# Optimization experiments

Measured on AMD Instinct MI355X. Metric: run time of the kernel, lower is better.

Reference implementation:

```python
import jax, jax.numpy as jnp
import numpy as np

H, P, N, D, T, MLPW, B = 64, 4, 16, 8, 64, 512, 2048
D_IN = 1 + H + P * H  # 321


def _linear_init(key, i, o):
    k1, k2 = jax.random.split(key)
    s = 1.0 / np.sqrt(i)
    W = jax.random.uniform(k1, (i, o), jnp.float32, -s, s)
    b = jax.random.uniform(k2, (o,), jnp.float32, -s, s)
    return W, b


def setup_inputs() -> dict:
    key = jax.random.key(0)
    ks = jax.random.split(key, 10)
    dims_f = [(D_IN, MLPW), (MLPW, MLPW), (MLPW, MLPW), (MLPW, H)]
    dims_g = [(D_IN, MLPW), (MLPW, MLPW), (MLPW, MLPW), (MLPW, H * N)]
    inp = {}
    for idx, (i, o) in enumerate(dims_f):
        W, b = _linear_init(ks[idx], i, o)
        inp[f"fW{idx}"], inp[f"fb{idx}"] = W, b
    for idx, (i, o) in enumerate(dims_g):
        W, b = _linear_init(ks[4 + idx], i, o)
        inp[f"gW{idx}"], inp[f"gb{idx}"] = W, b
    inp["rW"], inp["rb"] = _linear_init(ks[8], H, D)
    inp["ts"] = jnp.arange(T, dtype=jnp.float32)  # uniform grid, dt = 1
    inp["dbt"] = jax.random.normal(ks[9], (T - 1, B, N), jnp.float32)  # per-step randn noise
    inp["batch_size"] = B
    return inp


def _mlp(x, params):
    # Linear+ReLU stack, final Linear with tanh (tscale=1.0)
    for W, b in params[:-1]:
        x = jax.nn.relu(x @ W + b)
    W, b = params[-1]
    return jnp.tanh(x @ W + b)


def _forward(ts, dbt, fp, gp, rW, rb, batch_size):
    x0 = jnp.ones((batch_size, H), jnp.float32)  # fixed=True initial state
    dt = ts[1] - ts[0]  # dt_scale = 1
    hist = jnp.zeros((T, batch_size, H), jnp.float32).at[0].set(x0)
    curr_x, curr_t = x0, ts[0]
    xs = [x0]
    for k in range(T - 1):  # one integration step per output interval (uniform ts)
        # ortho rfft over the growing state history (length k+1); keep first P coeffs,
        # real part (matches torch complex -> .float() cast), zero-pad to P.
        coeffs = jnp.fft.rfft(hist[: k + 1], axis=0, norm="ortho")  # (F, B, H) complex
        c = jnp.real(coeffs[:P]).astype(jnp.float32)
        if c.shape[0] < P:
            c = jnp.concatenate(
                [c, jnp.zeros((P - c.shape[0], batch_size, H), jnp.float32)], axis=0
            )
        feats = jnp.transpose(c, (1, 0, 2)).reshape(batch_size, P * H)  # (B, P*H)
        tcol = jnp.broadcast_to(jnp.reshape(curr_t, (1, 1)), (batch_size, 1))
        tx = jnp.concatenate([tcol, curr_x, feats], axis=1)  # (B, 1+H+P*H)
        drift = _mlp(tx, fp)  # (B, H)
        diff = _mlp(tx, gp).reshape(batch_size, H, N)  # (B, H, N)
        curr_x = curr_x + drift * dt + jnp.einsum("bhn,bn->bh", diff, dbt[k])
        curr_t = jnp.minimum(curr_t + dt, ts[-1])
        hist = hist.at[k + 1].set(curr_x)
        xs.append(curr_x)  # linear_interp degenerates to curr_x on uniform grid
    xs = jnp.stack(xs, axis=1)  # (B, T, H)
    ys = xs @ rW + rb  # readout, (B, T, D)
    tse = jnp.broadcast_to(ts[None, :, None], (batch_size, T, 1))
    # linear_interpolation_coeffs is identity for NaN-free data
    return jnp.concatenate([tse, ys], axis=2)  # (B, T, 1+D)


def reference(fW0, fb0, fW1, fb1, fW2, fb2, fW3, fb3,
              gW0, gb0, gW1, gb1, gW2, gb2, gW3, gb3,
              rW, rb, ts, dbt, batch_size):
    fp = [(fW0, fb0), (fW1, fb1), (fW2, fb2), (fW3, fb3)]
    gp = [(gW0, gb0), (gW1, gb1), (gW2, gb2), (gW3, gb3)]
    return _forward(ts, dbt, fp, gp, rW, rb, batch_size)
```

## Files before the change

### kernel.cpp

```cpp
#include <hip/hip_runtime.h>
#include <math.h>

constexpr int kH   = 64;
constexpr int kP   = 4;
constexpr int kN   = 16;
constexpr int kD   = 8;
constexpr int kT   = 64;
constexpr int kWd  = 512;
constexpr int kB   = 2048;
constexpr int kDIN = 1 + kH + kP * kH;
constexpr int kKP  = 352;
constexpr int kBH  = kB * kH;

typedef __attribute__((ext_vector_type(8))) short short8;
typedef __attribute__((ext_vector_type(4))) float f32x4;

__device__ __forceinline__ short f2bf(float x) {
    union { float f; unsigned u; } v; v.f = x;
    unsigned r = (v.u + 0x7FFFu + ((v.u >> 16) & 1u)) >> 16;
    return (short)r;
}

__device__ __forceinline__ void gload16(const short* g, short* l) {
    __builtin_amdgcn_global_load_lds(
        (const __attribute__((address_space(1))) unsigned int*)g,
        (__attribute__((address_space(3))) unsigned int*)l, 16, 0, 0);
}

__global__ __launch_bounds__(256) void transpose_bf16(const float* __restrict__ W,
                                                      short* __restrict__ Wt,
                                                      int K, int N, int Kp, int Np) {
    int idx = blockIdx.x * 256 + threadIdx.x;
    if (idx >= Kp * Np) return;
    int n = idx / Kp, kk = idx % Kp;
    float v = (kk < K && n < N) ? W[(size_t)kk * N + n] : 0.f;
    Wt[idx] = f2bf(v);
}

__global__ __launch_bounds__(256) void prep_bias(const float* __restrict__ fb0,
                                                 const float* __restrict__ gb0,
                                                 float* __restrict__ b0c) {
    int i = blockIdx.x * 256 + threadIdx.x;
    if (i < 1024) b0c[i] = (i < kWd) ? fb0[i] : gb0[i - kWd];
}

__global__ __launch_bounds__(256) void init_k(float* __restrict__ hist,
                                              short* __restrict__ txh) {
    int idx = blockIdx.x * 256 + threadIdx.x;
    if (idx < kBH) hist[idx] = 1.0f;
    if (idx < kB * (kKP - kDIN)) {
        int b = idx / (kKP - kDIN), c = idx % (kKP - kDIN);
        txh[(size_t)b * kKP + kDIN + c] = 0;
    }
}

__global__ __launch_bounds__(256) void step_pre(float* __restrict__ hist,
                                                const float* __restrict__ drift,
                                                const float* __restrict__ diffb,
                                                const float* __restrict__ dbt,
                                                short* __restrict__ txh, int k) {
    const int L = k + 1;
    __shared__ float ctab[kT * kP];
    int tid = threadIdx.x;
    float invs = rsqrtf((float)L);
    for (int i = tid; i < L * kP; i += 256) {
        int j = i >> 2, p = i & 3;
        ctab[i] = cosf(6.283185307179586f * (float)(p * j) / (float)L) * invs;
    }
    __syncthreads();
    int idx = blockIdx.x * 256 + tid;
    int b = idx >> 6, h = idx & 63;
    float xk;
    if (k == 0) {
        xk = 1.0f;
    } else {
        xk = hist[(size_t)(k - 1) * kBH + idx] + drift[idx];
        const float* dr = diffb + (size_t)b * 1024 + h * kN;
        const float* wr = dbt + (size_t)(k - 1) * kB * kN + b * kN;
#pragma unroll
        for (int n = 0; n < kN; ++n) xk += dr[n] * wr[n];
        hist[(size_t)k * kBH + idx] = xk;
    }
    const float* hp = hist + (size_t)b * kH + h;
    float a0 = 0.f, a1 = 0.f, a2 = 0.f, a3 = 0.f;
    for (int j = 0; j < k; ++j) {
        float x = hp[(size_t)j * kBH];
        a0 += x * ctab[j * 4 + 0];
        a1 += x * ctab[j * 4 + 1];
        a2 += x * ctab[j * 4 + 2];
        a3 += x * ctab[j * 4 + 3];
    }
    a0 += xk * ctab[k * 4 + 0];
    a1 += xk * ctab[k * 4 + 1];
    a2 += xk * ctab[k * 4 + 2];
    a3 += xk * ctab[k * 4 + 3];
    if (L < 2) a1 = 0.f;
    if (L < 4) a2 = 0.f;
    if (L < 6) a3 = 0.f;
    short* th = txh + (size_t)b * kKP;
    th[1 + kH + 0 * kH + h] = f2bf(a0);
    th[1 + kH + 1 * kH + h] = f2bf(a1);
    th[1 + kH + 2 * kH + h] = f2bf(a2);
    th[1 + kH + 3 * kH + h] = f2bf(a3);
    th[1 + h] = f2bf(xk);
    if (h == 0) th[0] = f2bf((float)k);
}

struct MArg {
    const short* A;
    const short* Bt;
    const float* bias;
    short* Cb;
    float* Cf;
    int K, lda, ldc, act, Nw;
};

__global__ __launch_bounds__(256) void gemm_mfma(MArg f, MArg g, int ysplit) {
    const int y = blockIdx.y;
    MArg a;
    int n0;
    if (y < ysplit) { a = f; n0 = y * 64; }
    else            { a = g; n0 = (y - ysplit) * 64; }
    const int m0 = blockIdx.x * 64;

    __shared__ __align__(16) short sA[64 * 32];
    __shared__ __align__(16) short sB[64 * 32];

    const int tid = threadIdx.x;
    const int lane = tid & 63;
    const int w = tid >> 6;
    const int wm = (w & 1) * 32;
    const int wn = (w >> 1) * 32;

    f32x4 acc[2][2] = {};

    const int sr = tid >> 2;
    const int sc = (tid & 3) * 8;
    const short* gA = a.A  + (size_t)(m0 + sr) * a.lda + sc;
    const short* gB = a.Bt + (size_t)(n0 + sr) * a.K + sc;

    for (int k0 = 0; k0 < a.K; k0 += 32) {
        __syncthreads();
        gload16(gA + k0, &sA[sr * 32 + sc]);
        gload16(gB + k0, &sB[sr * 32 + sc]);
        __syncthreads();

        const int fr = lane & 15, kb = (lane >> 4) * 8;
        short8 av[2], bv[2];
#pragma unroll
        for (int i = 0; i < 2; ++i) {
            av[i] = *(const short8*)&sA[(wm + i * 16 + fr) * 32 + kb];
            bv[i] = *(const short8*)&sB[(wn + i * 16 + fr) * 32 + kb];
        }
#pragma unroll
        for (int i = 0; i < 2; ++i)
#pragma unroll
            for (int j = 0; j < 2; ++j)
                acc[i][j] = __builtin_amdgcn_mfma_f32_16x16x32_bf16(av[i], bv[j], acc[i][j], 0, 0, 0);
    }

    const int fr = lane & 15, rq = (lane >> 4) * 4;
#pragma unroll
    for (int j = 0; j < 2; ++j) {
        int n = n0 + wn + j * 16 + fr;
        if (n >= a.Nw) continue;
        float bias = a.bias[n];
#pragma unroll
        for (int i = 0; i < 2; ++i) {
#pragma unroll
            for (int r = 0; r < 4; ++r) {
                int m = m0 + wm + i * 16 + rq + r;
                float v = acc[i][j][r] + bias;
                if (a.act == 0) {
                    a.Cb[(size_t)m * a.ldc + n] = f2bf(fmaxf(v, 0.f));
                } else {
                    a.Cf[(size_t)m * a.ldc + n] = tanhf(v);
                }
            }
        }
    }
}

__global__ __launch_bounds__(256) void update_k(float* __restrict__ hist,
                                                const float* __restrict__ drift,
                                                const float* __restrict__ diffb,
                                                const float* __restrict__ dbt, int k) {
    int idx = blockIdx.x * 256 + threadIdx.x;
    int b = idx >> 6, h = idx & 63;
    float s = hist[(size_t)k * kBH + idx] + drift[idx];
    const float* dr = diffb + (size_t)b * 1024 + h * kN;
    const float* wr = dbt + (size_t)k * kB * kN + b * kN;
#pragma unroll
    for (int n = 0; n < kN; ++n) s += dr[n] * wr[n];
    hist[(size_t)(k + 1) * kBH + idx] = s;
}

__global__ __launch_bounds__(256) void readout_k(const float* __restrict__ hist,
                                                 const float* __restrict__ rW,
                                                 const float* __restrict__ rb,
                                                 const float* __restrict__ ts,
                                                 float* __restrict__ out) {
    __shared__ float sW[kH * kD];
    __shared__ float sb[kD];
    __shared__ float sts[kT];
    int tid = threadIdx.x;
    sW[tid] = rW[tid];
    sW[tid + 256] = rW[tid + 256];
    if (tid < kD) sb[tid] = rb[tid];
    if (tid < kT) sts[tid] = ts[tid];
    __syncthreads();
    int idx = blockIdx.x * 256 + tid;
    int t = idx & (kT - 1), b = idx >> 6;
    const float* xr = hist + (size_t)t * kBH + (size_t)b * kH;
    float acc[kD];
#pragma unroll
    for (int d = 0; d < kD; ++d) acc[d] = sb[d];
    for (int h = 0; h < kH; ++h) {
        float x = xr[h];
#pragma unroll
        for (int d = 0; d < kD; ++d) acc[d] += x * sW[h * kD + d];
    }
    float* o = out + (size_t)((size_t)b * kT + t) * (1 + kD);
    o[0] = sts[t];
#pragma unroll
    for (int d = 0; d < kD; ++d) o[1 + d] = acc[d];
}

extern "C" void kernel_launch(void* const* d_in, const int* in_sizes, int n_in,
                              void* d_out, int out_size, void* d_ws, size_t ws_size,
                              hipStream_t stream) {
    const float* fW0 = (const float*)d_in[0];  const float* fb0 = (const float*)d_in[1];
    const float* fW1 = (const float*)d_in[2];  const float* fb1 = (const float*)d_in[3];
    const float* fW2 = (const float*)d_in[4];  const float* fb2 = (const float*)d_in[5];
    const float* fW3 = (const float*)d_in[6];  const float* fb3 = (const float*)d_in[7];
    const float* gW0 = (const float*)d_in[8];  const float* gb0 = (const float*)d_in[9];
    const float* gW1 = (const float*)d_in[10]; const float* gb1 = (const float*)d_in[11];
    const float* gW2 = (const float*)d_in[12]; const float* gb2 = (const float*)d_in[13];
    const float* gW3 = (const float*)d_in[14]; const float* gb3 = (const float*)d_in[15];
    const float* rW  = (const float*)d_in[16]; const float* rb  = (const float*)d_in[17];
    const float* ts  = (const float*)d_in[18]; const float* dbt = (const float*)d_in[19];
    float* out = (float*)d_out;

    char* p = (char*)d_ws;
    float* hist  = (float*)p;  p += (size_t)kT * kBH * 4;
    float* drift = (float*)p;  p += (size_t)kBH * 4;
    float* diffb = (float*)p;  p += (size_t)kB * 1024 * 4;
    float* b0c   = (float*)p;  p += 1024 * 4;
    short* txh   = (short*)p;  p += (size_t)kB * kKP * 2;
    short* b1h   = (short*)p;  p += (size_t)kB * 1024 * 2;
    short* b2h   = (short*)p;  p += (size_t)kB * 1024 * 2;
    short* W0t   = (short*)p;  p += (size_t)1024 * kKP * 2;
    short* fW1t  = (short*)p;  p += (size_t)512 * 512 * 2;
    short* gW1t  = (short*)p;  p += (size_t)512 * 512 * 2;
    short* fW2t  = (short*)p;  p += (size_t)512 * 512 * 2;
    short* gW2t  = (short*)p;  p += (size_t)512 * 512 * 2;
    short* fW3t  = (short*)p;  p += (size_t)64 * 512 * 2;
    short* gW3t  = (short*)p;  p += (size_t)1024 * 512 * 2;

    auto tgrid = [](int n) { return dim3((n + 255) / 256); };
    transpose_bf16<<<tgrid(kKP * 512), 256, 0, stream>>>(fW0, W0t, kDIN, 512, kKP, 512);
    transpose_bf16<<<tgrid(kKP * 512), 256, 0, stream>>>(gW0, W0t + (size_t)512 * kKP, kDIN, 512, kKP, 512);
    transpose_bf16<<<tgrid(512 * 512), 256, 0, stream>>>(fW1, fW1t, 512, 512, 512, 512);
    transpose_bf16<<<tgrid(512 * 512), 256, 0, stream>>>(gW1, gW1t, 512, 512, 512, 512);
    transpose_bf16<<<tgrid(512 * 512), 256, 0, stream>>>(fW2, fW2t, 512, 512, 512, 512);
    transpose_bf16<<<tgrid(512 * 512), 256, 0, stream>>>(gW2, gW2t, 512, 512, 512, 512);
    transpose_bf16<<<tgrid(512 * 64), 256, 0, stream>>>(fW3, fW3t, 512, 64, 512, 64);
    transpose_bf16<<<tgrid(512 * 1024), 256, 0, stream>>>(gW3, gW3t, 512, 1024, 512, 1024);
    prep_bias<<<dim3(4), 256, 0, stream>>>(fb0, gb0, b0c);
    init_k<<<dim3(kBH / 256), 256, 0, stream>>>(hist, txh);

    for (int k = 0; k < kT - 1; ++k) {
        step_pre<<<dim3(kBH / 256), 256, 0, stream>>>(hist, drift, diffb, dbt, txh, k);

        MArg l1{txh, W0t, b0c, b1h, nullptr, kKP, kKP, 1024, 0, 1024};
        gemm_mfma<<<dim3(32, 16), 256, 0, stream>>>(l1, l1, 16);

        MArg f2{b1h, fW1t, fb1, b2h, nullptr, 512, 1024, 1024, 0, 512};
        MArg g2{b1h + 512, gW1t, gb1, b2h + 512, nullptr, 512, 1024, 1024, 0, 512};
        gemm_mfma<<<dim3(32, 16), 256, 0, stream>>>(f2, g2, 8);

        MArg f3{b2h, fW2t, fb2, b1h, nullptr, 512, 1024, 1024, 0, 512};
        MArg g3{b2h + 512, gW2t, gb2, b1h + 512, nullptr, 512, 1024, 1024, 0, 512};
        gemm_mfma<<<dim3(32, 16), 256, 0, stream>>>(f3, g3, 8);

        MArg f4{b1h, fW3t, fb3, nullptr, drift, 512, 1024, kH, 1, kH};
        MArg g4{b1h + 512, gW3t, gb3, nullptr, diffb, 512, 1024, 1024, 1, 1024};
        gemm_mfma<<<dim3(32, 17), 256, 0, stream>>>(f4, g4, 1);
    }

    update_k<<<dim3(kBH / 256), 256, 0, stream>>>(hist, drift, diffb, dbt, kT - 2);
    readout_k<<<dim3(kB * kT / 256), 256, 0, stream>>>(hist, rW, rb, ts, out);
}
```

Before: 2.943 ms.

## Double-buffer GEMM K-loop with swizzled LDS and store diffusion output as bf16

The MFMA GEMM now processes 64-wide K tiles split into two 32-wide halves, double-buffered in LDS so the next tile's global->LDS loads overlap with the current tile's MFMAs. LDS columns are XOR-swizzled to reduce bank conflicts. The padded input width grows to 384 so K is a multiple of 64, and launch bounds request two blocks per SM. The diffusion head output is stored as bf16 instead of fp32 to halve its traffic, at some precision cost in the state update.

Result: faster. 2.548 ms (-13.4%).

```diff
diff --git a/kernel.cpp b/kernel.cpp
--- a/kernel.cpp
+++ b/kernel.cpp
@@ -9,7 +9,7 @@
 constexpr int kWd  = 512;
 constexpr int kB   = 2048;
 constexpr int kDIN = 1 + kH + kP * kH;
-constexpr int kKP  = 352;
+constexpr int kKP  = 384;
 constexpr int kBH  = kB * kH;
 
 typedef __attribute__((ext_vector_type(8))) short short8;
@@ -19,6 +19,10 @@
     union { float f; unsigned u; } v; v.f = x;
     unsigned r = (v.u + 0x7FFFu + ((v.u >> 16) & 1u)) >> 16;
     return (short)r;
+}
+__device__ __forceinline__ float bf2f(short h) {
+    union { unsigned u; float f; } v; v.u = ((unsigned)(unsigned short)h) << 16;
+    return v.f;
 }
 
 __device__ __forceinline__ void gload16(const short* g, short* l) {
@@ -56,7 +60,7 @@
 
 __global__ __launch_bounds__(256) void step_pre(float* __restrict__ hist,
                                                 const float* __restrict__ drift,
-                                                const float* __restrict__ diffb,
+                                                const short* __restrict__ diffb,
                                                 const float* __restrict__ dbt,
                                                 short* __restrict__ txh, int k) {
     const int L = k + 1;
@@ -75,10 +79,10 @@
         xk = 1.0f;
     } else {
         xk = hist[(size_t)(k - 1) * kBH + idx] + drift[idx];
-        const float* dr = diffb + (size_t)b * 1024 + h * kN;
+        const short* dr = diffb + (size_t)b * 1024 + h * kN;
         const float* wr = dbt + (size_t)(k - 1) * kB * kN + b * kN;
 #pragma unroll
-        for (int n = 0; n < kN; ++n) xk += dr[n] * wr[n];
+        for (int n = 0; n < kN; ++n) xk += bf2f(dr[n]) * wr[n];
         hist[(size_t)k * kBH + idx] = xk;
     }
     const float* hp = hist + (size_t)b * kH + h;
@@ -115,7 +119,7 @@
     int K, lda, ldc, act, Nw;
 };
 
-__global__ __launch_bounds__(256) void gemm_mfma(MArg f, MArg g, int ysplit) {
+__global__ __launch_bounds__(256, 2) void gemm_mfma(MArg f, MArg g, int ysplit) {
     const int y = blockIdx.y;
     MArg a;
     int n0;
@@ -123,8 +127,8 @@
     else            { a = g; n0 = (y - ysplit) * 64; }
     const int m0 = blockIdx.x * 64;
 
-    __shared__ __align__(16) short sA[64 * 32];
-    __shared__ __align__(16) short sB[64 * 32];
+    __shared__ __align__(16) short sA[2][2][64 * 32];
+    __shared__ __align__(16) short sB[2][2][64 * 32];
 
     const int tid = threadIdx.x;
     const int lane = tid & 63;
@@ -132,34 +136,51 @@
     const int wm = (w & 1) * 32;
     const int wn = (w >> 1) * 32;
 
+    const int sr = tid >> 2;
+    const int s  = tid & 3;
+    const int scol = (s ^ ((sr >> 1) & 3)) * 8;
+    const int sdst = sr * 32 + s * 8;
+
+    const short* gA = a.A  + (size_t)(m0 + sr) * a.lda + scol;
+    const short* gB = a.Bt + (size_t)(n0 + sr) * a.K   + scol;
+
+    const int nk = a.K >> 6;
     f32x4 acc[2][2] = {};
 
-    const int sr = tid >> 2;
-    const int sc = (tid & 3) * 8;
-    const short* gA = a.A  + (size_t)(m0 + sr) * a.lda + sc;
-    const short* gB = a.Bt + (size_t)(n0 + sr) * a.K + sc;
-
-    for (int k0 = 0; k0 < a.K; k0 += 32) {
+    gload16(gA,      &sA[0][0][sdst]);
+    gload16(gA + 32, &sA[0][1][sdst]);
+    gload16(gB,      &sB[0][0][sdst]);
+    gload16(gB + 32, &sB[0][1][sdst]);
+
+    const int fr = lane & 15;
+    const int kb = ((lane >> 4) ^ ((fr >> 1) & 3)) * 8;
+    const int ra0 = (wm + fr) * 32 + kb, ra1 = (wm + 16 + fr) * 32 + kb;
+    const int rb0 = (wn + fr) * 32 + kb, rb1 = (wn + 16 + fr) * 32 + kb;
+
+    for (int kt = 0; kt < nk; ++kt) {
         __syncthreads();
-        gload16(gA + k0, &sA[sr * 32 + sc]);
-        gload16(gB + k0, &sB[sr * 32 + sc]);
-        __syncthreads();
-
-        const int fr = lane & 15, kb = (lane >> 4) * 8;
-        short8 av[2], bv[2];
-#pragma unroll
-        for (int i = 0; i < 2; ++i) {
-            av[i] = *(const short8*)&sA[(wm + i * 16 + fr) * 32 + kb];
-            bv[i] = *(const short8*)&sB[(wn + i * 16 + fr) * 32 + kb];
+        const int cur = kt & 1, nxt = cur ^ 1;
+        if (kt + 1 < nk) {
+            const int ko = (kt + 1) << 6;
+            gload16(gA + ko,      &sA[nxt][0][sdst]);
+            gload16(gA + ko + 32, &sA[nxt][1][sdst]);
+            gload16(gB + ko,      &sB[nxt][0][sdst]);
+            gload16(gB + ko + 32, &sB[nxt][1][sdst]);
         }
 #pragma unroll
-        for (int i = 0; i < 2; ++i)
-#pragma unroll
-            for (int j = 0; j < 2; ++j)
-                acc[i][j] = __builtin_amdgcn_mfma_f32_16x16x32_bf16(av[i], bv[j], acc[i][j], 0, 0, 0);
-    }
-
-    const int fr = lane & 15, rq = (lane >> 4) * 4;
+        for (int ks = 0; ks < 2; ++ks) {
+            short8 a0 = *(const short8*)&sA[cur][ks][ra0];
+            short8 a1 = *(const short8*)&sA[cur][ks][ra1];
+            short8 b0 = *(const short8*)&sB[cur][ks][rb0];
+            short8 b1 = *(const short8*)&sB[cur][ks][rb1];
+            acc[0][0] = __builtin_amdgcn_mfma_f32_16x16x32_bf16(a0, b0, acc[0][0], 0, 0, 0);
+            acc[0][1] = __builtin_amdgcn_mfma_f32_16x16x32_bf16(a0, b1, acc[0][1], 0, 0, 0);
+            acc[1][0] = __builtin_amdgcn_mfma_f32_16x16x32_bf16(a1, b0, acc[1][0], 0, 0, 0);
+            acc[1][1] = __builtin_amdgcn_mfma_f32_16x16x32_bf16(a1, b1, acc[1][1], 0, 0, 0);
+        }
+    }
+
+    const int rq = (lane >> 4) * 4;
 #pragma unroll
     for (int j = 0; j < 2; ++j) {
         int n = n0 + wn + j * 16 + fr;
@@ -173,6 +194,8 @@
                 float v = acc[i][j][r] + bias;
                 if (a.act == 0) {
                     a.Cb[(size_t)m * a.ldc + n] = f2bf(fmaxf(v, 0.f));
+                } else if (a.Cb) {
+                    a.Cb[(size_t)m * a.ldc + n] = f2bf(tanhf(v));
                 } else {
                     a.Cf[(size_t)m * a.ldc + n] = tanhf(v);
                 }
@@ -183,15 +206,15 @@
 
 __global__ __launch_bounds__(256) void update_k(float* __restrict__ hist,
                                                 const float* __restrict__ drift,
-                                                const float* __restrict__ diffb,
+                                                const short* __restrict__ diffb,
                                                 const float* __restrict__ dbt, int k) {
     int idx = blockIdx.x * 256 + threadIdx.x;
     int b = idx >> 6, h = idx & 63;
     float s = hist[(size_t)k * kBH + idx] + drift[idx];
-    const float* dr = diffb + (size_t)b * 1024 + h * kN;
+    const short* dr = diffb + (size_t)b * 1024 + h * kN;
     const float* wr = dbt + (size_t)k * kB * kN + b * kN;
 #pragma unroll
-    for (int n = 0; n < kN; ++n) s += dr[n] * wr[n];
+    for (int n = 0; n < kN; ++n) s += bf2f(dr[n]) * wr[n];
     hist[(size_t)(k + 1) * kBH + idx] = s;
 }
 
@@ -244,8 +267,8 @@
     char* p = (char*)d_ws;
     float* hist  = (float*)p;  p += (size_t)kT * kBH * 4;
     float* drift = (float*)p;  p += (size_t)kBH * 4;
-    float* diffb = (float*)p;  p += (size_t)kB * 1024 * 4;
     float* b0c   = (float*)p;  p += 1024 * 4;
+    short* diffb = (short*)p;  p += (size_t)kB * 1024 * 2;
     short* txh   = (short*)p;  p += (size_t)kB * kKP * 2;
     short* b1h   = (short*)p;  p += (size_t)kB * 1024 * 2;
     short* b2h   = (short*)p;  p += (size_t)kB * 1024 * 2;
@@ -284,7 +307,7 @@
         gemm_mfma<<<dim3(32, 16), 256, 0, stream>>>(f3, g3, 8);
 
         MArg f4{b1h, fW3t, fb3, nullptr, drift, 512, 1024, kH, 1, kH};
-        MArg g4{b1h + 512, gW3t, gb3, nullptr, diffb, 512, 1024, 1024, 1, 1024};
+        MArg g4{b1h + 512, gW3t, gb3, diffb, nullptr, 512, 1024, 1024, 1, 1024};
         gemm_mfma<<<dim3(32, 17), 256, 0, stream>>>(f4, g4, 1);
     }
 
```

## Fuse per-step feature build and full MLP stack into one persistent-tile kernel

Applied to the files above, without the earlier changes.

Replaces the five launches per time step (feature prep plus four GEMM layers) with one kernel. Each block owns 32 batch rows and one branch (drift or diffusion) and keeps the activations in swizzled LDS across all layers, reading weights directly from global memory with register prefetch. The diffusion-noise contraction is folded into the last layer's epilogue through lane shuffles, and the history is also stored in bf16 to cut the FFT-feature reads. Drift and delta buffers are double-buffered across steps. The cost is that every block rereads the full weight matrices from global or L2 memory, and only 128 blocks of 1024 threads run.

Result: slower. 7.783 ms (+164.5%).

```diff
diff --git a/kernel.cpp b/kernel.cpp
--- a/kernel.cpp
+++ b/kernel.cpp
@@ -9,8 +9,9 @@
 constexpr int kWd  = 512;
 constexpr int kB   = 2048;
 constexpr int kDIN = 1 + kH + kP * kH;
-constexpr int kKP  = 352;
+constexpr int kKP  = 384;
 constexpr int kBH  = kB * kH;
+constexpr int kMT  = 32;
 
 typedef __attribute__((ext_vector_type(8))) short short8;
 typedef __attribute__((ext_vector_type(4))) float f32x4;
@@ -20,11 +21,14 @@
     unsigned r = (v.u + 0x7FFFu + ((v.u >> 16) & 1u)) >> 16;
     return (short)r;
 }
-
-__device__ __forceinline__ void gload16(const short* g, short* l) {
-    __builtin_amdgcn_global_load_lds(
-        (const __attribute__((address_space(1))) unsigned int*)g,
-        (__attribute__((address_space(3))) unsigned int*)l, 16, 0, 0);
+__device__ __forceinline__ float bf2f(short h) {
+    union { unsigned u; float f; } v; v.u = ((unsigned)(unsigned short)h) << 16;
+    return v.f;
+}
+
+__device__ __forceinline__ int swzi(int row, int col, int stride) {
+    int slot = col >> 3;
+    return row * stride + ((slot ^ (row & 7)) << 3) + (col & 7);
 }
 
 __global__ __launch_bounds__(256) void transpose_bf16(const float* __restrict__ W,
@@ -37,162 +41,242 @@
     Wt[idx] = f2bf(v);
 }
 
-__global__ __launch_bounds__(256) void prep_bias(const float* __restrict__ fb0,
-                                                 const float* __restrict__ gb0,
-                                                 float* __restrict__ b0c) {
-    int i = blockIdx.x * 256 + threadIdx.x;
-    if (i < 1024) b0c[i] = (i < kWd) ? fb0[i] : gb0[i - kWd];
-}
-
-__global__ __launch_bounds__(256) void init_k(float* __restrict__ hist,
-                                              short* __restrict__ txh) {
-    int idx = blockIdx.x * 256 + threadIdx.x;
-    if (idx < kBH) hist[idx] = 1.0f;
-    if (idx < kB * (kKP - kDIN)) {
-        int b = idx / (kKP - kDIN), c = idx % (kKP - kDIN);
-        txh[(size_t)b * kKP + kDIN + c] = 0;
-    }
-}
-
-__global__ __launch_bounds__(256) void step_pre(float* __restrict__ hist,
-                                                const float* __restrict__ drift,
-                                                const float* __restrict__ diffb,
-                                                const float* __restrict__ dbt,
-                                                short* __restrict__ txh, int k) {
+template <int KDIM>
+__device__ __forceinline__ void mlp_layer(const short* __restrict__ sIn,
+                                          const short* __restrict__ Bt,
+                                          const float* __restrict__ bias,
+                                          short* __restrict__ sOut, int tid) {
+    const int w = tid >> 6, lane = tid & 63;
+    const int wm = (w & 1) * 16, wn = (w >> 1) * 64;
+    const int frc = lane & 15, kq = lane >> 4;
+    const int nk = KDIM / 32;
+
+    const short* bp0 = Bt + (size_t)(wn + 0 * 16 + frc) * KDIM + kq * 8;
+    const short* bp1 = Bt + (size_t)(wn + 1 * 16 + frc) * KDIM + kq * 8;
+    const short* bp2 = Bt + (size_t)(wn + 2 * 16 + frc) * KDIM + kq * 8;
+    const short* bp3 = Bt + (size_t)(wn + 3 * 16 + frc) * KDIM + kq * 8;
+
+    f32x4 acc[4] = {};
+    short8 b0 = *(const short8*)bp0, b1 = *(const short8*)bp1;
+    short8 b2 = *(const short8*)bp2, b3 = *(const short8*)bp3;
+
+    const int arow = wm + frc;
+    const short* aBase = sIn + arow * KDIM;
+    const int amask = arow & 7;
+
+    for (int kt = 0; kt < nk; ++kt) {
+        short8 n0, n1, n2, n3;
+        if (kt + 1 < nk) {
+            n0 = *(const short8*)(bp0 + (kt + 1) * 32);
+            n1 = *(const short8*)(bp1 + (kt + 1) * 32);
+            n2 = *(const short8*)(bp2 + (kt + 1) * 32);
+            n3 = *(const short8*)(bp3 + (kt + 1) * 32);
+        }
+        short8 av = *(const short8*)(aBase + (((kt * 4 + kq) ^ amask) << 3));
+        acc[0] = __builtin_amdgcn_mfma_f32_16x16x32_bf16(av, b0, acc[0], 0, 0, 0);
+        acc[1] = __builtin_amdgcn_mfma_f32_16x16x32_bf16(av, b1, acc[1], 0, 0, 0);
+        acc[2] = __builtin_amdgcn_mfma_f32_16x16x32_bf16(av, b2, acc[2], 0, 0, 0);
+        acc[3] = __builtin_amdgcn_mfma_f32_16x16x32_bf16(av, b3, acc[3], 0, 0, 0);
+        b0 = n0; b1 = n1; b2 = n2; b3 = n3;
+    }
+
+    const int rq = (lane >> 4) * 4;
+#pragma unroll
+    for (int j = 0; j < 4; ++j) {
+        int n = wn + j * 16 + frc;
+        float bv = bias[n];
+#pragma unroll
+        for (int r = 0; r < 4; ++r) {
+            int row = wm + rq + r;
+            sOut[swzi(row, n, 512)] = f2bf(fmaxf(acc[j][r] + bv, 0.f));
+        }
+    }
+}
+
+__global__ __launch_bounds__(1024) void fused_step(
+    float* __restrict__ hist, short* __restrict__ histb,
+    const float* __restrict__ driftR, const float* __restrict__ xdeltaR,
+    float* __restrict__ driftW, float* __restrict__ xdeltaW,
+    const float* __restrict__ dbt,
+    const short* __restrict__ W0t, const float* __restrict__ fb0,
+    const float* __restrict__ gb0,
+    const short* __restrict__ fW1t, const float* __restrict__ fb1,
+    const short* __restrict__ gW1t, const float* __restrict__ gb1,
+    const short* __restrict__ fW2t, const float* __restrict__ fb2,
+    const short* __restrict__ gW2t, const float* __restrict__ gb2,
+    const short* __restrict__ fW3t, const float* __restrict__ fb3,
+    const short* __restrict__ gW3t, const float* __restrict__ gb3,
+    int k) {
+    __shared__ __align__(16) short sTX[kMT * kKP];
+    __shared__ __align__(16) short sA1[kMT * 512];
+    __shared__ __align__(16) short sA2[kMT * 512];
+    __shared__ float ctab[kT * kP];
+    __shared__ float sdb[kMT * kN];
+
+    const int bid = blockIdx.x;
+    const int gbr = bid & 1;
+    const int m0 = (bid >> 1) * kMT;
+    const int tid = threadIdx.x;
     const int L = k + 1;
-    __shared__ float ctab[kT * kP];
-    int tid = threadIdx.x;
-    float invs = rsqrtf((float)L);
-    for (int i = tid; i < L * kP; i += 256) {
-        int j = i >> 2, p = i & 3;
-        ctab[i] = cosf(6.283185307179586f * (float)(p * j) / (float)L) * invs;
-    }
-    __syncthreads();
-    int idx = blockIdx.x * 256 + tid;
-    int b = idx >> 6, h = idx & 63;
-    float xk;
-    if (k == 0) {
-        xk = 1.0f;
-    } else {
-        xk = hist[(size_t)(k - 1) * kBH + idx] + drift[idx];
-        const float* dr = diffb + (size_t)b * 1024 + h * kN;
-        const float* wr = dbt + (size_t)(k - 1) * kB * kN + b * kN;
-#pragma unroll
-        for (int n = 0; n < kN; ++n) xk += dr[n] * wr[n];
-        hist[(size_t)k * kBH + idx] = xk;
-    }
-    const float* hp = hist + (size_t)b * kH + h;
-    float a0 = 0.f, a1 = 0.f, a2 = 0.f, a3 = 0.f;
-    for (int j = 0; j < k; ++j) {
-        float x = hp[(size_t)j * kBH];
-        a0 += x * ctab[j * 4 + 0];
-        a1 += x * ctab[j * 4 + 1];
-        a2 += x * ctab[j * 4 + 2];
-        a3 += x * ctab[j * 4 + 3];
-    }
-    a0 += xk * ctab[k * 4 + 0];
-    a1 += xk * ctab[k * 4 + 1];
-    a2 += xk * ctab[k * 4 + 2];
-    a3 += xk * ctab[k * 4 + 3];
-    if (L < 2) a1 = 0.f;
-    if (L < 4) a2 = 0.f;
-    if (L < 6) a3 = 0.f;
-    short* th = txh + (size_t)b * kKP;
-    th[1 + kH + 0 * kH + h] = f2bf(a0);
-    th[1 + kH + 1 * kH + h] = f2bf(a1);
-    th[1 + kH + 2 * kH + h] = f2bf(a2);
-    th[1 + kH + 3 * kH + h] = f2bf(a3);
-    th[1 + h] = f2bf(xk);
-    if (h == 0) th[0] = f2bf((float)k);
-}
-
-struct MArg {
-    const short* A;
-    const short* Bt;
-    const float* bias;
-    short* Cb;
-    float* Cf;
-    int K, lda, ldc, act, Nw;
-};
-
-__global__ __launch_bounds__(256) void gemm_mfma(MArg f, MArg g, int ysplit) {
-    const int y = blockIdx.y;
-    MArg a;
-    int n0;
-    if (y < ysplit) { a = f; n0 = y * 64; }
-    else            { a = g; n0 = (y - ysplit) * 64; }
-    const int m0 = blockIdx.x * 64;
-
-    __shared__ __align__(16) short sA[64 * 32];
-    __shared__ __align__(16) short sB[64 * 32];
-
-    const int tid = threadIdx.x;
-    const int lane = tid & 63;
-    const int w = tid >> 6;
-    const int wm = (w & 1) * 32;
-    const int wn = (w >> 1) * 32;
-
-    f32x4 acc[2][2] = {};
-
-    const int sr = tid >> 2;
-    const int sc = (tid & 3) * 8;
-    const short* gA = a.A  + (size_t)(m0 + sr) * a.lda + sc;
-    const short* gB = a.Bt + (size_t)(n0 + sr) * a.K + sc;
-
-    for (int k0 = 0; k0 < a.K; k0 += 32) {
-        __syncthreads();
-        gload16(gA + k0, &sA[sr * 32 + sc]);
-        gload16(gB + k0, &sB[sr * 32 + sc]);
-        __syncthreads();
-
-        const int fr = lane & 15, kb = (lane >> 4) * 8;
-        short8 av[2], bv[2];
-#pragma unroll
-        for (int i = 0; i < 2; ++i) {
-            av[i] = *(const short8*)&sA[(wm + i * 16 + fr) * 32 + kb];
-            bv[i] = *(const short8*)&sB[(wn + i * 16 + fr) * 32 + kb];
-        }
-#pragma unroll
-        for (int i = 0; i < 2; ++i)
-#pragma unroll
-            for (int j = 0; j < 2; ++j)
-                acc[i][j] = __builtin_amdgcn_mfma_f32_16x16x32_bf16(av[i], bv[j], acc[i][j], 0, 0, 0);
-    }
-
-    const int fr = lane & 15, rq = (lane >> 4) * 4;
-#pragma unroll
-    for (int j = 0; j < 2; ++j) {
-        int n = n0 + wn + j * 16 + fr;
-        if (n >= a.Nw) continue;
-        float bias = a.bias[n];
-#pragma unroll
-        for (int i = 0; i < 2; ++i) {
-#pragma unroll
-            for (int r = 0; r < 4; ++r) {
-                int m = m0 + wm + i * 16 + rq + r;
-                float v = acc[i][j][r] + bias;
-                if (a.act == 0) {
-                    a.Cb[(size_t)m * a.ldc + n] = f2bf(fmaxf(v, 0.f));
-                } else {
-                    a.Cf[(size_t)m * a.ldc + n] = tanhf(v);
+
+    if (tid < L * 4) {
+        int j = tid >> 2, p = tid & 3;
+        ctab[tid] = cosf(6.283185307179586f * (float)(p * j) / (float)L) *
+                    rsqrtf((float)L);
+    }
+    if (gbr && tid < kMT * kN)
+        sdb[tid] = dbt[((size_t)k * kB + m0) * kN + tid];
+    __syncthreads();
+
+#pragma unroll
+    for (int pass = 0; pass < 2; ++pass) {
+        int idx = pass * 1024 + tid;
+        int row = idx >> 6, h = idx & 63;
+        int bg = m0 + row;
+        float xk;
+        if (k == 0) {
+            xk = 1.0f;
+        } else {
+            xk = hist[(size_t)(k - 1) * kBH + bg * 64 + h] +
+                 driftR[bg * 64 + h] + xdeltaR[bg * 64 + h];
+        }
+        if (!gbr) {
+            hist[(size_t)k * kBH + bg * 64 + h] = xk;
+            histb[(size_t)k * kBH + bg * 64 + h] = f2bf(xk);
+        }
+        float a0 = 0.f, a1 = 0.f, a2 = 0.f, a3 = 0.f;
+        const short* hb = histb + (size_t)bg * 64 + h;
+        for (int j = 0; j < k; ++j) {
+            float x = bf2f(hb[(size_t)j * kBH]);
+            a0 += x * ctab[j * 4 + 0];
+            a1 += x * ctab[j * 4 + 1];
+            a2 += x * ctab[j * 4 + 2];
+            a3 += x * ctab[j * 4 + 3];
+        }
+        a0 += xk * ctab[k * 4 + 0];
+        a1 += xk * ctab[k * 4 + 1];
+        a2 += xk * ctab[k * 4 + 2];
+        a3 += xk * ctab[k * 4 + 3];
+        if (L < 2) a1 = 0.f;
+        if (L < 4) a2 = 0.f;
+        if (L < 6) a3 = 0.f;
+        sTX[swzi(row, 1 + h, kKP)] = f2bf(xk);
+        sTX[swzi(row, 65 + 0 * 64 + h, kKP)] = f2bf(a0);
+        sTX[swzi(row, 65 + 1 * 64 + h, kKP)] = f2bf(a1);
+        sTX[swzi(row, 65 + 2 * 64 + h, kKP)] = f2bf(a2);
+        sTX[swzi(row, 65 + 3 * 64 + h, kKP)] = f2bf(a3);
+        if (h == 0) sTX[swzi(row, 0, kKP)] = f2bf((float)k);
+        if (h < 63) sTX[swzi(row, 321 + h, kKP)] = 0;
+    }
+    __syncthreads();
+
+    mlp_layer<kKP>(sTX, W0t + (size_t)(gbr ? 512 : 0) * kKP,
+                   gbr ? gb0 : fb0, sA1, tid);
+    __syncthreads();
+    mlp_layer<512>(sA1, gbr ? gW1t : fW1t, gbr ? gb1 : fb1, sA2, tid);
+    __syncthreads();
+    mlp_layer<512>(sA2, gbr ? gW2t : fW2t, gbr ? gb2 : fb2, sA1, tid);
+    __syncthreads();
+
+    const int w = tid >> 6, lane = tid & 63;
+    const int frc = lane & 15, kq = lane >> 4;
+    const int rq = kq * 4;
+
+    if (!gbr) {
+        if (w < 2) {
+            const int wm = w * 16;
+            const short* bp0 = fW3t + (size_t)(0 * 16 + frc) * 512 + kq * 8;
+            const short* bp1 = fW3t + (size_t)(1 * 16 + frc) * 512 + kq * 8;
+            const short* bp2 = fW3t + (size_t)(2 * 16 + frc) * 512 + kq * 8;
+            const short* bp3 = fW3t + (size_t)(3 * 16 + frc) * 512 + kq * 8;
+            f32x4 acc[4] = {};
+            const int arow = wm + frc;
+            const short* aBase = sA1 + arow * 512;
+            const int amask = arow & 7;
+            for (int kt = 0; kt < 16; ++kt) {
+                short8 av = *(const short8*)(aBase + (((kt * 4 + kq) ^ amask) << 3));
+                short8 b0 = *(const short8*)(bp0 + kt * 32);
+                short8 b1 = *(const short8*)(bp1 + kt * 32);
+                short8 b2 = *(const short8*)(bp2 + kt * 32);
+                short8 b3 = *(const short8*)(bp3 + kt * 32);
+                acc[0] = __builtin_amdgcn_mfma_f32_16x16x32_bf16(av, b0, acc[0], 0, 0, 0);
+                acc[1] = __builtin_amdgcn_mfma_f32_16x16x32_bf16(av, b1, acc[1], 0, 0, 0);
+                acc[2] = __builtin_amdgcn_mfma_f32_16x16x32_bf16(av, b2, acc[2], 0, 0, 0);
+                acc[3] = __builtin_amdgcn_mfma_f32_16x16x32_bf16(av, b3, acc[3], 0, 0, 0);
+            }
+#pragma unroll
+            for (int j = 0; j < 4; ++j) {
+                int n = j * 16 + frc;
+                float bv = fb3[n];
+#pragma unroll
+                for (int r = 0; r < 4; ++r) {
+                    int row = wm + rq + r;
+                    driftW[(size_t)(m0 + row) * 64 + n] = tanhf(acc[j][r] + bv);
                 }
             }
         }
+    } else {
+        const int wn = w * 64;
+        const short* bp0 = gW3t + (size_t)(wn + 0 * 16 + frc) * 512 + kq * 8;
+        const short* bp1 = gW3t + (size_t)(wn + 1 * 16 + frc) * 512 + kq * 8;
+        const short* bp2 = gW3t + (size_t)(wn + 2 * 16 + frc) * 512 + kq * 8;
+        const short* bp3 = gW3t + (size_t)(wn + 3 * 16 + frc) * 512 + kq * 8;
+        f32x4 acc[2][4] = {};
+        const short* aB0 = sA1 + (0 * 16 + frc) * 512;
+        const short* aB1 = sA1 + (16 + frc) * 512;
+        const int am0 = frc & 7, am1 = (16 + frc) & 7;
+        short8 b0 = *(const short8*)bp0, b1 = *(const short8*)bp1;
+        short8 b2 = *(const short8*)bp2, b3 = *(const short8*)bp3;
+        for (int kt = 0; kt < 16; ++kt) {
+            short8 n0, n1, n2, n3;
+            if (kt < 15) {
+                n0 = *(const short8*)(bp0 + (kt + 1) * 32);
+                n1 = *(const short8*)(bp1 + (kt + 1) * 32);
+                n2 = *(const short8*)(bp2 + (kt + 1) * 32);
+                n3 = *(const short8*)(bp3 + (kt + 1) * 32);
+            }
+            short8 a0v = *(const short8*)(aB0 + (((kt * 4 + kq) ^ am0) << 3));
+            short8 a1v = *(const short8*)(aB1 + (((kt * 4 + kq) ^ am1) << 3));
+            acc[0][0] = __builtin_amdgcn_mfma_f32_16x16x32_bf16(a0v, b0, acc[0][0], 0, 0, 0);
+            acc[0][1] = __builtin_amdgcn_mfma_f32_16x16x32_bf16(a0v, b1, acc[0][1], 0, 0, 0);
+            acc[0][2] = __builtin_amdgcn_mfma_f32_16x16x32_bf16(a0v, b2, acc[0][2], 0, 0, 0);
+            acc[0][3] = __builtin_amdgcn_mfma_f32_16x16x32_bf16(a0v, b3, acc[0][3], 0, 0, 0);
+            acc[1][0] = __builtin_amdgcn_mfma_f32_16x16x32_bf16(a1v, b0, acc[1][0], 0, 0, 0);
+            acc[1][1] = __builtin_amdgcn_mfma_f32_16x16x32_bf16(a1v, b1, acc[1][1], 0, 0, 0);
+            acc[1][2] = __builtin_amdgcn_mfma_f32_16x16x32_bf16(a1v, b2, acc[1][2], 0, 0, 0);
+            acc[1][3] = __builtin_amdgcn_mfma_f32_16x16x32_bf16(a1v, b3, acc[1][3], 0, 0, 0);
+            b0 = n0; b1 = n1; b2 = n2; b3 = n3;
+        }
+#pragma unroll
+        for (int j = 0; j < 4; ++j) {
+            int n = wn + j * 16 + frc;
+            float bv = gb3[n];
+            int h = (w << 2) + j;
+#pragma unroll
+            for (int i = 0; i < 2; ++i) {
+#pragma unroll
+                for (int r = 0; r < 4; ++r) {
+                    int row = i * 16 + rq + r;
+                    float v = tanhf(acc[i][j][r] + bv);
+                    float p = v * sdb[row * 16 + frc];
+                    p += __shfl_xor(p, 1);
+                    p += __shfl_xor(p, 2);
+                    p += __shfl_xor(p, 4);
+                    p += __shfl_xor(p, 8);
+                    if (frc == 0)
+                        xdeltaW[(size_t)(m0 + row) * 64 + h] = p;
+                }
+            }
+        }
     }
 }
 
 __global__ __launch_bounds__(256) void update_k(float* __restrict__ hist,
                                                 const float* __restrict__ drift,
-                                                const float* __restrict__ diffb,
-                                                const float* __restrict__ dbt, int k) {
+                                                const float* __restrict__ xdelta, int k) {
     int idx = blockIdx.x * 256 + threadIdx.x;
-    int b = idx >> 6, h = idx & 63;
-    float s = hist[(size_t)k * kBH + idx] + drift[idx];
-    const float* dr = diffb + (size_t)b * 1024 + h * kN;
-    const float* wr = dbt + (size_t)k * kB * kN + b * kN;
-#pragma unroll
-    for (int n = 0; n < kN; ++n) s += dr[n] * wr[n];
-    hist[(size_t)(k + 1) * kBH + idx] = s;
+    hist[(size_t)(k + 1) * kBH + idx] =
+        hist[(size_t)k * kBH + idx] + drift[idx] + xdelta[idx];
 }
 
 __global__ __launch_bounds__(256) void readout_k(const float* __restrict__ hist,
@@ -242,20 +326,19 @@
     float* out = (float*)d_out;
 
     char* p = (char*)d_ws;
-    float* hist  = (float*)p;  p += (size_t)kT * kBH * 4;
-    float* drift = (float*)p;  p += (size_t)kBH * 4;
-    float* diffb = (float*)p;  p += (size_t)kB * 1024 * 4;
-    float* b0c   = (float*)p;  p += 1024 * 4;
-    short* txh   = (short*)p;  p += (size_t)kB * kKP * 2;
-    short* b1h   = (short*)p;  p += (size_t)kB * 1024 * 2;
-    short* b2h   = (short*)p;  p += (size_t)kB * 1024 * 2;
-    short* W0t   = (short*)p;  p += (size_t)1024 * kKP * 2;
-    short* fW1t  = (short*)p;  p += (size_t)512 * 512 * 2;
-    short* gW1t  = (short*)p;  p += (size_t)512 * 512 * 2;
-    short* fW2t  = (short*)p;  p += (size_t)512 * 512 * 2;
-    short* gW2t  = (short*)p;  p += (size_t)512 * 512 * 2;
-    short* fW3t  = (short*)p;  p += (size_t)64 * 512 * 2;
-    short* gW3t  = (short*)p;  p += (size_t)1024 * 512 * 2;
+    float* hist   = (float*)p;  p += (size_t)kT * kBH * 4;
+    short* histb  = (short*)p;  p += (size_t)(kT - 1) * kBH * 2;
+    float* drift0 = (float*)p;  p += (size_t)kBH * 4;
+    float* drift1 = (float*)p;  p += (size_t)kBH * 4;
+    float* xdel0  = (float*)p;  p += (size_t)kBH * 4;
+    float* xdel1  = (float*)p;  p += (size_t)kBH * 4;
+    short* W0t    = (short*)p;  p += (size_t)1024 * kKP * 2;
+    short* fW1t   = (short*)p;  p += (size_t)512 * 512 * 2;
+    short* gW1t   = (short*)p;  p += (size_t)512 * 512 * 2;
+    short* fW2t   = (short*)p;  p += (size_t)512 * 512 * 2;
+    short* gW2t   = (short*)p;  p += (size_t)512 * 512 * 2;
+    short* fW3t   = (short*)p;  p += (size_t)64 * 512 * 2;
+    short* gW3t   = (short*)p;  p += (size_t)1024 * 512 * 2;
 
     auto tgrid = [](int n) { return dim3((n + 255) / 256); };
     transpose_bf16<<<tgrid(kKP * 512), 256, 0, stream>>>(fW0, W0t, kDIN, 512, kKP, 512);
@@ -266,28 +349,17 @@
     transpose_bf16<<<tgrid(512 * 512), 256, 0, stream>>>(gW2, gW2t, 512, 512, 512, 512);
     transpose_bf16<<<tgrid(512 * 64), 256, 0, stream>>>(fW3, fW3t, 512, 64, 512, 64);
     transpose_bf16<<<tgrid(512 * 1024), 256, 0, stream>>>(gW3, gW3t, 512, 1024, 512, 1024);
-    prep_bias<<<dim3(4), 256, 0, stream>>>(fb0, gb0, b0c);
-    init_k<<<dim3(kBH / 256), 256, 0, stream>>>(hist, txh);
 
     for (int k = 0; k < kT - 1; ++k) {
-        step_pre<<<dim3(kBH / 256), 256, 0, stream>>>(hist, drift, diffb, dbt, txh, k);
-
-        MArg l1{txh, W0t, b0c, b1h, nullptr, kKP, kKP, 1024, 0, 1024};
-        gemm_mfma<<<dim3(32, 16), 256, 0, stream>>>(l1, l1, 16);
-
-        MArg f2{b1h, fW1t, fb1, b2h, nullptr, 512, 1024, 1024, 0, 512};
-        MArg g2{b1h + 512, gW1t, gb1, b2h + 512, nullptr, 512, 1024, 1024, 0, 512};
-        gemm_mfma<<<dim3(32, 16), 256, 0, stream>>>(f2, g2, 8);
-
-        MArg f3{b2h, fW2t, fb2, b1h, nullptr, 512, 1024, 1024, 0, 512};
-        MArg g3{b2h + 512, gW2t, gb2, b1h + 512, nullptr, 512, 1024, 1024, 0, 512};
-        gemm_mfma<<<dim3(32, 16), 256, 0, stream>>>(f3, g3, 8);
-
-        MArg f4{b1h, fW3t, fb3, nullptr, drift, 512, 1024, kH, 1, kH};
-        MArg g4{b1h + 512, gW3t, gb3, nullptr, diffb, 512, 1024, 1024, 1, 1024};
-        gemm_mfma<<<dim3(32, 17), 256, 0, stream>>>(f4, g4, 1);
-    }
-
-    update_k<<<dim3(kBH / 256), 256, 0, stream>>>(hist, drift, diffb, dbt, kT - 2);
+        const int par = k & 1;
+        fused_step<<<dim3(kB / kMT * 2), 1024, 0, stream>>>(
+            hist, histb,
+            par ? drift0 : drift1, par ? xdel0 : xdel1,
+            par ? drift1 : drift0, par ? xdel1 : xdel0,
+            dbt, W0t, fb0, gb0, fW1t, fb1, gW1t, gb1,
+            fW2t, fb2, gW2t, gb2, fW3t, fb3, gW3t, gb3, k);
+    }
+
+    update_k<<<dim3(kBH / 256), 256, 0, stream>>>(hist, drift0, xdel0, kT - 2);
     readout_k<<<dim3(kB * kT / 256), 256, 0, stream>>>(hist, rW, rb, ts, out);
 }
```
